# Performance work log

Hardware: AMD Instinct MI355X
Metric: run time of the kernel (lower is better)

Reference implementation:

```python
import jax, jax.numpy as jnp
import numpy as np

N_HEADS = 8
MAX_PARTS = 8
TOKENS_PER_PART = 64
NUM_BLOCKS = 6
D_MODEL = 256
LN_EPS = 1e-5


def layernorm(x, w, b):
    mu = jnp.mean(x, axis=-1, keepdims=True)
    var = jnp.var(x, axis=-1, keepdims=True)
    return (x - mu) * jax.lax.rsqrt(var + LN_EPS) * w + b


def mha(q, k, v, in_w, in_b, out_w, out_b):
    # torch nn.MultiheadAttention: packed in_proj [3D, D], out_proj [D, D]
    D = q.shape[-1]
    dh = D // N_HEADS
    wq, wk, wv = in_w[:D], in_w[D:2 * D], in_w[2 * D:]
    bq, bk, bv = in_b[:D], in_b[D:2 * D], in_b[2 * D:]
    qp = q @ wq.T + bq  # [B, Sq, D]
    kp = k @ wk.T + bk
    vp = v @ wv.T + bv
    B, Sq, _ = qp.shape
    Sk = kp.shape[1]
    qh = qp.reshape(B, Sq, N_HEADS, dh).transpose(0, 2, 1, 3)
    kh = kp.reshape(B, Sk, N_HEADS, dh).transpose(0, 2, 1, 3)
    vh = vp.reshape(B, Sk, N_HEADS, dh).transpose(0, 2, 1, 3)
    scores = jnp.einsum('bhqd,bhkd->bhqk', qh, kh) / jnp.sqrt(jnp.asarray(dh, qp.dtype))
    attn = jax.nn.softmax(scores, axis=-1)
    out = jnp.einsum('bhqk,bhkd->bhqd', attn, vh)
    out = out.transpose(0, 2, 1, 3).reshape(B, Sq, D)
    return out @ out_w.T + out_b


def setup_inputs() -> dict:
    key = jax.random.key(0)
    ks = jax.random.split(key, 16)
    s = 0.02
    return {
        'feat': jax.random.normal(ks[0], (64, 49, 512), jnp.float32),
        'img_proj_w': jax.random.normal(ks[1], (256, 512), jnp.float32) * s,
        'img_proj_b': jnp.zeros((256,), jnp.float32),
        'init_part_tokens': jax.random.normal(ks[2], (512, 256), jnp.float32),
        'part_id_emb': jax.random.normal(ks[3], (8, 256), jnp.float32),
        'local_in_w': jax.random.normal(ks[4], (768, 256), jnp.float32) * s,
        'local_in_b': jnp.zeros((768,), jnp.float32),
        'local_out_w': jax.random.normal(ks[5], (256, 256), jnp.float32) * s,
        'local_out_b': jnp.zeros((256,), jnp.float32),
        'cross_in_w': jax.random.normal(ks[6], (768, 256), jnp.float32) * s,
        'cross_in_b': jnp.zeros((768,), jnp.float32),
        'cross_out_w': jax.random.normal(ks[7], (256, 256), jnp.float32) * s,
        'cross_out_b': jnp.zeros((256,), jnp.float32),
        'norm1_w': jnp.ones((6, 256), jnp.float32),
        'norm1_b': jnp.zeros((6, 256), jnp.float32),
        'norm2_w': jnp.ones((6, 256), jnp.float32),
        'norm2_b': jnp.zeros((6, 256), jnp.float32),
        'coord_w': jax.random.normal(ks[8], (3, 256), jnp.float32) * s,
        'coord_b': jnp.zeros((3,), jnp.float32),
    }


def reference(feat, img_proj_w, img_proj_b, init_part_tokens, part_id_emb,
              local_in_w, local_in_b, local_out_w, local_out_b,
              cross_in_w, cross_in_b, cross_out_w, cross_out_b,
              norm1_w, norm1_b, norm2_w, norm2_b, coord_w, coord_b):
    B = feat.shape[0]
    P, T, D = MAX_PARTS, TOKENS_PER_PART, D_MODEL
    img_tokens = feat @ img_proj_w.T + img_proj_b  # [B, 49, D]
    # broadcast part-id embedding over tokens_per_part
    pid = jnp.repeat(part_id_emb, T, axis=0)  # [P*T, D]
    st = jnp.broadcast_to(init_part_tokens + pid, (B, P * T, D))
    for i in range(NUM_BLOCKS):
        # block-diagonal local attention: fold parts into batch dim
        parts = st.reshape(B * P, T, D)
        local = mha(parts, parts, parts, local_in_w, local_in_b, local_out_w, local_out_b)
        local = local.reshape(B, P * T, D)
        st = layernorm(st + local, norm1_w[i], norm1_b[i])
        cross = mha(st, img_tokens, img_tokens, cross_in_w, cross_in_b, cross_out_w, cross_out_b)
        st = layernorm(st + cross, norm2_w[i], norm2_b[i])
    coords = st @ coord_w.T + coord_b
    return coords.reshape(B, P, T, 3)
```

## Files before the change

kernel.cpp:

```cpp
#include <hip/hip_runtime.h>
#include <hip/hip_bf16.h>


#define B_     64
#define P_     8
#define T_     64
#define S_     512
#define D_     256
#define H_     8
#define DH_    32
#define NIMG_  49
#define M_ST   32768
#define M_IMG  3136
#define OSTR   264

#define AS1 __attribute__((address_space(1)))
#define AS3 __attribute__((address_space(3)))

typedef short bf16x8 __attribute__((ext_vector_type(8)));
typedef float f32x4  __attribute__((ext_vector_type(4)));

__device__ inline uint f2b_pk(float x, float y) {
    uint bx = __float_as_uint(x), by = __float_as_uint(y);
    bx = (bx + 0x7FFFu + ((bx >> 16) & 1u)) >> 16;
    by = (by + 0x7FFFu + ((by >> 16) & 1u)) >> 16;
    return bx | (by << 16);
}
__device__ inline ushort f2b(float x) {
    uint b = __float_as_uint(x);
    return (ushort)((b + 0x7FFFu + ((b >> 16) & 1u)) >> 16);
}
__device__ inline float b2f(ushort u) {
    return __uint_as_float(((uint)u) << 16);
}

__global__ __launch_bounds__(256) void cvt_bf16x4(
    const float4* __restrict__ in, uint2* __restrict__ out, int n4)
{
    int i = blockIdx.x * 256 + threadIdx.x;
    if (i < n4) {
        float4 v = in[i];
        out[i] = make_uint2(f2b_pk(v.x, v.y), f2b_pk(v.z, v.w));
    }
}

__global__ __launch_bounds__(256) void gemm_bf16(
    const ushort* __restrict__ A,
    const ushort* __restrict__ W,
    const float*  __restrict__ bias,
    ushort*       __restrict__ C,
    int M, int N, int K)
{
    __shared__ ushort smem[128 * 128];
    ushort* Asm = smem;
    ushort* Bsm = smem + 4096;

    const int tid  = threadIdx.x;
    const int lane = tid & 63;
    const int wave = tid >> 6;
    const int wr = wave >> 1, wc = wave & 1;
    const int row0 = blockIdx.x * 128, col0 = blockIdx.y * 128;

    f32x4 acc[4][4] = {};

    const int skc = (tid & 3) * 8;
    const int sr0 = tid >> 2;
    const int fr  = lane & 15;
    const int g   = lane >> 4;

    for (int k0 = 0; k0 < K; k0 += 32) {
        #pragma unroll
        for (int i = 0; i < 2; ++i) {
            const int r = sr0 + i * 64;
            const int e = (tid + i * 256) * 8;
            int ra = row0 + r; if (ra >= M) ra = M - 1;
            __builtin_amdgcn_global_load_lds(
                (const AS1 void*)(A + (size_t)ra * K + k0 + skc),
                (AS3 void*)&Asm[e], 16, 0, 0);
            __builtin_amdgcn_global_load_lds(
                (const AS1 void*)(W + (size_t)(col0 + r) * K + k0 + skc),
                (AS3 void*)&Bsm[e], 16, 0, 0);
        }
        __syncthreads();

        bf16x8 af[4], bf[4];
        #pragma unroll
        for (int i = 0; i < 4; ++i)
            af[i] = *reinterpret_cast<const bf16x8*>(&Asm[(wr * 64 + i * 16 + fr) * 32 + g * 8]);
        #pragma unroll
        for (int j = 0; j < 4; ++j)
            bf[j] = *reinterpret_cast<const bf16x8*>(&Bsm[(wc * 64 + j * 16 + fr) * 32 + g * 8]);
        #pragma unroll
        for (int i = 0; i < 4; ++i)
            #pragma unroll
            for (int j = 0; j < 4; ++j)
                acc[i][j] = __builtin_amdgcn_mfma_f32_16x16x32_bf16(
                    af[i], bf[j], acc[i][j], 0, 0, 0);
        __syncthreads();
    }

    float bn[4];
    #pragma unroll
    for (int j = 0; j < 4; ++j) bn[j] = bias[col0 + wc * 64 + j * 16 + fr];

    #pragma unroll
    for (int i = 0; i < 4; ++i)
        #pragma unroll
        for (int j = 0; j < 4; ++j)
            #pragma unroll
            for (int r = 0; r < 4; ++r)
                smem[(wr * 64 + i * 16 + g * 4 + r) * 128 + wc * 64 + j * 16 + fr] =
                    f2b(acc[i][j][r] + bn[j]);
    __syncthreads();

    #pragma unroll
    for (int it = 0; it < 8; ++it) {
        const int elem = (it * 256 + tid) * 8;
        const int lrow = elem >> 7, lcol = elem & 127;
        const int m = row0 + lrow;
        if (m < M)
            *reinterpret_cast<uint4*>(&C[(size_t)m * N + col0 + lcol]) =
                *reinterpret_cast<const uint4*>(&smem[elem]);
    }
}

__global__ __launch_bounds__(256) void gemm_bf16_a32(
    const float*  __restrict__ A,
    const ushort* __restrict__ W,
    const float*  __restrict__ bias,
    ushort*       __restrict__ C,
    int M, int N, int K)
{
    __shared__ ushort smem[128 * 128];
    ushort* Asm = smem;
    ushort* Bsm = smem + 4096;

    const int tid  = threadIdx.x;
    const int lane = tid & 63;
    const int wave = tid >> 6;
    const int wr = wave >> 1, wc = wave & 1;
    const int row0 = blockIdx.x * 128, col0 = blockIdx.y * 128;

    f32x4 acc[4][4] = {};

    const int skc = (tid & 3) * 8;
    const int sr0 = tid >> 2;
    const int fr  = lane & 15;
    const int g   = lane >> 4;

    for (int k0 = 0; k0 < K; k0 += 32) {
        #pragma unroll
        for (int i = 0; i < 2; ++i) {
            const int r = sr0 + i * 64;
            const int e = (tid + i * 256) * 8;
            int ra = row0 + r; if (ra >= M) ra = M - 1;
            const float* ga = A + (size_t)ra * K + k0 + skc;
            float4 v0 = *reinterpret_cast<const float4*>(ga);
            float4 v1 = *reinterpret_cast<const float4*>(ga + 4);
            uint4 pk;
            pk.x = f2b_pk(v0.x, v0.y);
            pk.y = f2b_pk(v0.z, v0.w);
            pk.z = f2b_pk(v1.x, v1.y);
            pk.w = f2b_pk(v1.z, v1.w);
            *reinterpret_cast<uint4*>(&Asm[e]) = pk;
            __builtin_amdgcn_global_load_lds(
                (const AS1 void*)(W + (size_t)(col0 + r) * K + k0 + skc),
                (AS3 void*)&Bsm[e], 16, 0, 0);
        }
        __syncthreads();

        bf16x8 af[4], bf[4];
        #pragma unroll
        for (int i = 0; i < 4; ++i)
            af[i] = *reinterpret_cast<const bf16x8*>(&Asm[(wr * 64 + i * 16 + fr) * 32 + g * 8]);
        #pragma unroll
        for (int j = 0; j < 4; ++j)
            bf[j] = *reinterpret_cast<const bf16x8*>(&Bsm[(wc * 64 + j * 16 + fr) * 32 + g * 8]);
        #pragma unroll
        for (int i = 0; i < 4; ++i)
            #pragma unroll
            for (int j = 0; j < 4; ++j)
                acc[i][j] = __builtin_amdgcn_mfma_f32_16x16x32_bf16(
                    af[i], bf[j], acc[i][j], 0, 0, 0);
        __syncthreads();
    }

    float bn[4];
    #pragma unroll
    for (int j = 0; j < 4; ++j) bn[j] = bias[col0 + wc * 64 + j * 16 + fr];

    #pragma unroll
    for (int i = 0; i < 4; ++i)
        #pragma unroll
        for (int j = 0; j < 4; ++j)
            #pragma unroll
            for (int r = 0; r < 4; ++r)
                smem[(wr * 64 + i * 16 + g * 4 + r) * 128 + wc * 64 + j * 16 + fr] =
                    f2b(acc[i][j][r] + bn[j]);
    __syncthreads();

    #pragma unroll
    for (int it = 0; it < 8; ++it) {
        const int elem = (it * 256 + tid) * 8;
        const int lrow = elem >> 7, lcol = elem & 127;
        const int m = row0 + lrow;
        if (m < M)
            *reinterpret_cast<uint4*>(&C[(size_t)m * N + col0 + lcol]) =
                *reinterpret_cast<const uint4*>(&smem[elem]);
    }
}

__global__ __launch_bounds__(512, 4) void gemm_bf16_big(
    const ushort* __restrict__ A,
    const ushort* __restrict__ W,
    const float*  __restrict__ bias,
    ushort*       __restrict__ C,
    int N, int K)
{
    __shared__ ushort smem[16384];
    ushort* Asm = smem;
    ushort* Bsm = smem + 8192;

    const int tid  = threadIdx.x;
    const int lane = tid & 63;
    const int wave = tid >> 6;
    const int wr = wave >> 1, wc = wave & 1;
    const int row0 = blockIdx.x * 256, col0 = blockIdx.y * 128;

    f32x4 acc[4][4] = {};
    const int skc = (tid & 3) * 8;
    const int sr0 = tid >> 2;
    const int fr  = lane & 15;
    const int g   = lane >> 4;

    for (int k0 = 0; k0 < K; k0 += 32) {
        #pragma unroll
        for (int i = 0; i < 2; ++i) {
            const int r = sr0 + i * 128;
            __builtin_amdgcn_global_load_lds(
                (const AS1 void*)(A + (size_t)(row0 + r) * K + k0 + skc),
                (AS3 void*)&Asm[(tid + i * 512) * 8], 16, 0, 0);
        }
        __builtin_amdgcn_global_load_lds(
            (const AS1 void*)(W + (size_t)(col0 + sr0) * K + k0 + skc),
            (AS3 void*)&Bsm[tid * 8], 16, 0, 0);
        __syncthreads();

        bf16x8 af[4], bf[4];
        #pragma unroll
        for (int i = 0; i < 4; ++i)
            af[i] = *reinterpret_cast<const bf16x8*>(&Asm[(wr * 64 + i * 16 + fr) * 32 + g * 8]);
        #pragma unroll
        for (int j = 0; j < 4; ++j)
            bf[j] = *reinterpret_cast<const bf16x8*>(&Bsm[(wc * 64 + j * 16 + fr) * 32 + g * 8]);
        #pragma unroll
        for (int i = 0; i < 4; ++i)
            #pragma unroll
            for (int j = 0; j < 4; ++j)
                acc[i][j] = __builtin_amdgcn_mfma_f32_16x16x32_bf16(
                    af[i], bf[j], acc[i][j], 0, 0, 0);
        __syncthreads();
    }

    float bn[4];
    #pragma unroll
    for (int j = 0; j < 4; ++j) bn[j] = bias[col0 + wc * 64 + j * 16 + fr];

    #pragma unroll
    for (int h2 = 0; h2 < 2; ++h2) {
        if ((wr >> 1) == h2) {
            const int lwr = wr & 1;
            #pragma unroll
            for (int i = 0; i < 4; ++i)
                #pragma unroll
                for (int j = 0; j < 4; ++j)
                    #pragma unroll
                    for (int r = 0; r < 4; ++r)
                        smem[(lwr * 64 + i * 16 + g * 4 + r) * 128 + wc * 64 + j * 16 + fr] =
                            f2b(acc[i][j][r] + bn[j]);
        }
        __syncthreads();
        #pragma unroll
        for (int it = 0; it < 4; ++it) {
            const int elem = (it * 512 + tid) * 8;
            const int lrow = elem >> 7, lcol = elem & 127;
            *reinterpret_cast<uint4*>(
                &C[(size_t)(row0 + h2 * 128 + lrow) * N + col0 + lcol]) =
                *reinterpret_cast<const uint4*>(&smem[elem]);
        }
        __syncthreads();
    }
}

template<int CROSS>
__global__ __launch_bounds__(256) void attn_oln(
    const ushort* __restrict__ qsrc,
    const ushort* __restrict__ ksrc,
    const ushort* __restrict__ vsrc,
    const ushort* __restrict__ W,
    const float*  __restrict__ bias,
    ushort*       __restrict__ stb,
    const float*  __restrict__ lnw,
    const float*  __restrict__ lnb)
{
    constexpr int QSTR = CROSS ? 256 : 768;
    constexpr int KSTR = CROSS ? 512 : 768;

    const int bid = blockIdx.x;
    int qrow0, krow0;
    if (CROSS) { qrow0 = (bid >> 3) * 512 + (bid & 7) * 64; krow0 = (bid >> 3) * 49; }
    else       { qrow0 = bid * 64; krow0 = bid * 64; }

    __shared__ ushort P_lds[4][64][72];
    __shared__ ushort Vt_lds[4][32][72];
    __shared__ float  redS[64][4];
    __shared__ float  redS2[64][4];
    ushort* Os = &P_lds[0][0][0];

    const int tid = threadIdx.x;
    const int w = tid >> 6, l = tid & 63;
    const int fr = l & 15, g = l >> 4;
    ushort (*P)[72]  = P_lds[w];
    ushort (*Vt)[72] = Vt_lds[w];

    f32x4 o2[2][4][2] = {};

    #pragma unroll
    for (int hh = 0; hh < 2; ++hh) {
        const int h = w + hh * 4;
        const int hoff = h * 32;

        bf16x8 kf[4], qf[4];
        #pragma unroll
        for (int i = 0; i < 4; ++i) {
            int t = 16 * i + fr;
            if (CROSS && t > 48) t = 48;
            kf[i] = *reinterpret_cast<const bf16x8*>(
                ksrc + (size_t)(krow0 + t) * KSTR + hoff + g * 8);
        }
        #pragma unroll
        for (int j = 0; j < 4; ++j)
            qf[j] = *reinterpret_cast<const bf16x8*>(
                qsrc + (size_t)(qrow0 + 16 * j + fr) * QSTR + hoff + g * 8);

        #pragma unroll
        for (int t2 = 0; t2 < 2; ++t2) {
            const int task = t2 * 64 + l;
            const int rp = task >> 2, cg = task & 3;
            int r0 = 2 * rp, r1 = r0 + 1;
            if (CROSS) { if (r0 > 48) r0 = 48; if (r1 > 48) r1 = 48; }
            const uint4 a = *reinterpret_cast<const uint4*>(
                vsrc + (size_t)(krow0 + r0) * KSTR + hoff + cg * 8);
            const uint4 b = *reinterpret_cast<const uint4*>(
                vsrc + (size_t)(krow0 + r1) * KSTR + hoff + cg * 8);
            const uint ac[4] = {a.x, a.y, a.z, a.w};
            const uint bc[4] = {b.x, b.y, b.z, b.w};
            #pragma unroll
            for (int k = 0; k < 4; ++k) {
                uint lo = (ac[k] & 0xFFFFu) | (bc[k] << 16);
                uint hi = (ac[k] >> 16)     | (bc[k] & 0xFFFF0000u);
                *reinterpret_cast<uint*>(&Vt[cg * 8 + 2 * k][2 * rp])     = lo;
                *reinterpret_cast<uint*>(&Vt[cg * 8 + 2 * k + 1][2 * rp]) = hi;
            }
        }

        f32x4 st_[4][4];
        #pragma unroll
        for (int i = 0; i < 4; ++i)
            #pragma unroll
            for (int j = 0; j < 4; ++j) {
                f32x4 z = {};
                st_[i][j] = __builtin_amdgcn_mfma_f32_16x16x32_bf16(
                    kf[i], qf[j], z, 0, 0, 0);
                st_[i][j] *= 0.17677669529663689f;
            }
        if (CROSS) {
            #pragma unroll
            for (int j = 0; j < 4; ++j)
                #pragma unroll
                for (int r = 0; r < 4; ++r)
                    if (r > 0 || g > 0) st_[3][j][r] = -1e30f;
        }

        #pragma unroll
        for (int j = 0; j < 4; ++j) {
            float mx = -1e30f;
            #pragma unroll
            for (int i = 0; i < 4; ++i)
                #pragma unroll
                for (int r = 0; r < 4; ++r) mx = fmaxf(mx, st_[i][j][r]);
            mx = fmaxf(mx, __shfl_xor(mx, 16));
            mx = fmaxf(mx, __shfl_xor(mx, 32));
            float sm = 0.f;
            #pragma unroll
            for (int i = 0; i < 4; ++i)
                #pragma unroll
                for (int r = 0; r < 4; ++r) {
                    float p = __expf(st_[i][j][r] - mx);
                    st_[i][j][r] = p;
                    sm += p;
                }
            sm += __shfl_xor(sm, 16);
            sm += __shfl_xor(sm, 32);
            const float inv = 1.f / sm;
            const int q = 16 * j + fr;
            #pragma unroll
            for (int i = 0; i < 4; ++i) {
                uint lo = f2b_pk(st_[i][j][0] * inv, st_[i][j][1] * inv);
                uint hi = f2b_pk(st_[i][j][2] * inv, st_[i][j][3] * inv);
                *reinterpret_cast<uint2*>(&P[q][16 * i + 4 * g]) = make_uint2(lo, hi);
            }
        }

        __syncthreads();

        #pragma unroll
        for (int s = 0; s < 2; ++s) {
            bf16x8 pa[4], vb[2];
            #pragma unroll
            for (int i = 0; i < 4; ++i)
                pa[i] = *reinterpret_cast<const bf16x8*>(&P[16 * i + fr][32 * s + 8 * g]);
            #pragma unroll
            for (int j2 = 0; j2 < 2; ++j2)
                vb[j2] = *reinterpret_cast<const bf16x8*>(&Vt[16 * j2 + fr][32 * s + 8 * g]);
            #pragma unroll
            for (int i = 0; i < 4; ++i)
                #pragma unroll
                for (int j2 = 0; j2 < 2; ++j2)
                    o2[hh][i][j2] = __builtin_amdgcn_mfma_f32_16x16x32_bf16(
                        pa[i], vb[j2], o2[hh][i][j2], 0, 0, 0);
        }
    }

    __syncthreads();

    #pragma unroll
    for (int hh = 0; hh < 2; ++hh)
        #pragma unroll
        for (int i = 0; i < 4; ++i)
            #pragma unroll
            for (int j2 = 0; j2 < 2; ++j2)
                #pragma unroll
                for (int r = 0; r < 4; ++r)
                    Os[(16 * i + 4 * g + r) * OSTR + hh * 128 + w * 32 + 16 * j2 + fr] =
                        f2b(o2[hh][i][j2][r]);
    __syncthreads();

    f32x4 acc[4][4] = {};
    #pragma unroll
    for (int k0i = 0; k0i < 8; ++k0i) {
        const int k0 = k0i * 32;
        bf16x8 af[4], bf[4];
        #pragma unroll
        for (int j = 0; j < 4; ++j)
            bf[j] = *reinterpret_cast<const bf16x8*>(
                W + (size_t)(w * 64 + j * 16 + fr) * 256 + k0 + g * 8);
        #pragma unroll
        for (int i = 0; i < 4; ++i)
            af[i] = *reinterpret_cast<const bf16x8*>(&Os[(i * 16 + fr) * OSTR + k0 + g * 8]);
        #pragma unroll
        for (int i = 0; i < 4; ++i)
            #pragma unroll
            for (int j = 0; j < 4; ++j)
                acc[i][j] = __builtin_amdgcn_mfma_f32_16x16x32_bf16(
                    af[i], bf[j], acc[i][j], 0, 0, 0);
    }

    int   col[4]; float bv[4], wv[4], lb[4];
    #pragma unroll
    for (int j = 0; j < 4; ++j) {
        col[j] = w * 64 + j * 16 + fr;
        bv[j]  = bias[col[j]];
        wv[j]  = lnw[col[j]];
        lb[j]  = lnb[col[j]];
    }

    const int row0 = qrow0;

    #pragma unroll
    for (int i = 0; i < 4; ++i)
        #pragma unroll
        for (int r = 0; r < 4; ++r) {
            const int rl = i * 16 + g * 4 + r;
            const size_t rb = (size_t)(row0 + rl) * 256;
            float s = 0.f, s2 = 0.f;
            #pragma unroll
            for (int j = 0; j < 4; ++j) {
                float x = acc[i][j][r] + bv[j] + b2f(stb[rb + col[j]]);
                acc[i][j][r] = x;
                s += x; s2 += x * x;
            }
            #pragma unroll
            for (int o = 1; o < 16; o <<= 1) {
                s  += __shfl_xor(s, o);
                s2 += __shfl_xor(s2, o);
            }
            if (fr == 0) { redS[rl][w] = s; redS2[rl][w] = s2; }
        }
    __syncthreads();

    #pragma unroll
    for (int i = 0; i < 4; ++i)
        #pragma unroll
        for (int r = 0; r < 4; ++r) {
            const int rl = i * 16 + g * 4 + r;
            const float ts  = redS[rl][0] + redS[rl][1] + redS[rl][2] + redS[rl][3];
            const float ts2 = redS2[rl][0] + redS2[rl][1] + redS2[rl][2] + redS2[rl][3];
            const float mean = ts * (1.f / 256.f);
            const float var  = ts2 * (1.f / 256.f) - mean * mean;
            const float rs   = rsqrtf(var + 1e-5f);
            #pragma unroll
            for (int j = 0; j < 4; ++j) {
                const float y = (acc[i][j][r] - mean) * rs * wv[j] + lb[j];
                Os[rl * OSTR + col[j]] = f2b(y);
            }
        }
    __syncthreads();

    #pragma unroll
    for (int it = 0; it < 8; ++it) {
        const int e = it * 256 + tid;
        const int lrow = e >> 5, lcol = (e & 31) * 8;
        *reinterpret_cast<uint4*>(&stb[(size_t)(row0 + lrow) * 256 + lcol]) =
            *reinterpret_cast<const uint4*>(&Os[lrow * OSTR + lcol]);
    }
}

__global__ __launch_bounds__(256) void init_st(
    ushort* __restrict__ stb,
    const float* __restrict__ init_tokens, const float* __restrict__ pid_emb)
{
    int i = blockIdx.x * 256 + threadIdx.x;
    int c = i & 63;
    int s = (i >> 6) & 511;
    int p = s >> 6;
    float4 v = *reinterpret_cast<const float4*>(&init_tokens[s * 256 + c * 4]);
    float4 e = *reinterpret_cast<const float4*>(&pid_emb[p * 256 + c * 4]);
    v.x += e.x; v.y += e.y; v.z += e.z; v.w += e.w;
    *reinterpret_cast<uint2*>(&stb[(size_t)i * 4]) =
        make_uint2(f2b_pk(v.x, v.y), f2b_pk(v.z, v.w));
}

__global__ __launch_bounds__(256) void coord_head(
    const ushort* __restrict__ stb, const float* __restrict__ w,
    const float* __restrict__ b, float* __restrict__ out)
{
    const int row = blockIdx.x * 8 + (threadIdx.x >> 5);
    const int l   = threadIdx.x & 31;
    const ushort* x = stb + (size_t)row * 256 + l * 8;
    uint4 xv = *reinterpret_cast<const uint4*>(x);
    float xf[8];
    const uint xc[4] = {xv.x, xv.y, xv.z, xv.w};
    #pragma unroll
    for (int k = 0; k < 4; ++k) {
        xf[2*k]   = __uint_as_float(xc[k] << 16);
        xf[2*k+1] = __uint_as_float(xc[k] & 0xFFFF0000u);
    }
    float acc[3];
    #pragma unroll
    for (int n = 0; n < 3; ++n) {
        const float* wn = w + n * 256 + l * 8;
        float4 w0 = *reinterpret_cast<const float4*>(wn);
        float4 w1 = *reinterpret_cast<const float4*>(wn + 4);
        acc[n] = xf[0]*w0.x + xf[1]*w0.y + xf[2]*w0.z + xf[3]*w0.w
               + xf[4]*w1.x + xf[5]*w1.y + xf[6]*w1.z + xf[7]*w1.w;
    }
    #pragma unroll
    for (int o = 16; o; o >>= 1)
        #pragma unroll
        for (int n = 0; n < 3; ++n) acc[n] += __shfl_xor(acc[n], o);
    if (l == 0) {
        #pragma unroll
        for (int n = 0; n < 3; ++n) out[(size_t)row * 3 + n] = acc[n] + b[n];
    }
}

extern "C" void kernel_launch(void* const* d_in, const int* in_sizes, int n_in,
                              void* d_out, int out_size, void* d_ws, size_t ws_size,
                              hipStream_t stream)
{
    const float* feat             = (const float*)d_in[0];
    const float* img_proj_w      = (const float*)d_in[1];
    const float* img_proj_b      = (const float*)d_in[2];
    const float* init_part_tokens = (const float*)d_in[3];
    const float* part_id_emb     = (const float*)d_in[4];
    const float* local_in_w      = (const float*)d_in[5];
    const float* local_in_b      = (const float*)d_in[6];
    const float* local_out_w     = (const float*)d_in[7];
    const float* local_out_b     = (const float*)d_in[8];
    const float* cross_in_w      = (const float*)d_in[9];
    const float* cross_in_b      = (const float*)d_in[10];
    const float* cross_out_w     = (const float*)d_in[11];
    const float* cross_out_b     = (const float*)d_in[12];
    const float* norm1_w         = (const float*)d_in[13];
    const float* norm1_b         = (const float*)d_in[14];
    const float* norm2_w         = (const float*)d_in[15];
    const float* norm2_b         = (const float*)d_in[16];
    const float* coord_w         = (const float*)d_in[17];
    const float* coord_b         = (const float*)d_in[18];
    float* out = (float*)d_out;

    ushort* stb  = (ushort*)d_ws;
    ushort* big  = stb  + (size_t)M_ST * D_;
    ushort* kv   = big  + (size_t)M_ST * 3 * D_;
    ushort* img  = kv   + (size_t)M_IMG * 512;
    ushort* lw_in  = img   + (size_t)M_IMG * D_;
    ushort* lw_out = lw_in  + 768 * 256;
    ushort* cw_in  = lw_out + 256 * 256;
    ushort* cw_out = cw_in  + 768 * 256;
    ushort* iw     = cw_out + 256 * 256;

    cvt_bf16x4<<<768*256/4/256, 256, 0, stream>>>((const float4*)local_in_w,  (uint2*)lw_in,  768*256/4);
    cvt_bf16x4<<<256*256/4/256, 256, 0, stream>>>((const float4*)local_out_w, (uint2*)lw_out, 256*256/4);
    cvt_bf16x4<<<768*256/4/256, 256, 0, stream>>>((const float4*)cross_in_w,  (uint2*)cw_in,  768*256/4);
    cvt_bf16x4<<<256*256/4/256, 256, 0, stream>>>((const float4*)cross_out_w, (uint2*)cw_out, 256*256/4);
    cvt_bf16x4<<<256*512/4/256, 256, 0, stream>>>((const float4*)img_proj_w,  (uint2*)iw,     256*512/4);

    gemm_bf16_a32<<<dim3((M_IMG+127)/128, 2), 256, 0, stream>>>(
        feat, iw, img_proj_b, img, M_IMG, 256, 512);
    gemm_bf16<<<dim3((M_IMG+127)/128, 4), 256, 0, stream>>>(
        img, cw_in + 256*256, cross_in_b + 256, kv, M_IMG, 512, 256);
    init_st<<<M_ST * D_ / 4 / 256, 256, 0, stream>>>(stb, init_part_tokens, part_id_emb);

    for (int i = 0; i < 6; ++i) {
        gemm_bf16_big<<<dim3(M_ST/256, 6), 512, 0, stream>>>(stb, lw_in, local_in_b, big, 768, 256);
        attn_oln<0><<<512, 256, 0, stream>>>(big, big + 256, big + 512,
                                             lw_out, local_out_b, stb,
                                             norm1_w + i*256, norm1_b + i*256);
        gemm_bf16_big<<<dim3(M_ST/256, 2), 512, 0, stream>>>(stb, cw_in, cross_in_b, big, 256, 256);
        attn_oln<1><<<512, 256, 0, stream>>>(big, kv, kv + 256,
                                             cw_out, cross_out_b, stb,
                                             norm2_w + i*256, norm2_b + i*256);
    }

    coord_head<<<M_ST / 8, 256, 0, stream>>>(stb, coord_w, coord_b, out);
}
```

Measured before the change: 665.0 us.

## Fuse cross-attention Q projection into the attention kernel

```diff
diff --git a/kernel.cpp b/kernel.cpp
--- a/kernel.cpp
+++ b/kernel.cpp
@@ -297,6 +297,8 @@
     const ushort* __restrict__ qsrc,
     const ushort* __restrict__ ksrc,
     const ushort* __restrict__ vsrc,
+    const ushort* __restrict__ qw,
+    const float*  __restrict__ qb,
     const ushort* __restrict__ W,
     const float*  __restrict__ bias,
     ushort*       __restrict__ stb,
@@ -323,6 +325,56 @@
     ushort (*P)[72]  = P_lds[w];
     ushort (*Vt)[72] = Vt_lds[w];
 
+    bf16x8 qfA[2][4];
+    if constexpr (CROSS) {
+        f32x4 aq[4][4] = {};
+        #pragma unroll
+        for (int k0i = 0; k0i < 8; ++k0i) {
+            const int k0 = k0i * 32;
+            bf16x8 af[4], bf[4];
+            #pragma unroll
+            for (int i = 0; i < 4; ++i)
+                af[i] = *reinterpret_cast<const bf16x8*>(
+                    qsrc + (size_t)(qrow0 + i * 16 + fr) * 256 + k0 + g * 8);
+            #pragma unroll
+            for (int j = 0; j < 4; ++j)
+                bf[j] = *reinterpret_cast<const bf16x8*>(
+                    qw + (size_t)(w * 64 + j * 16 + fr) * 256 + k0 + g * 8);
+            #pragma unroll
+            for (int i = 0; i < 4; ++i)
+                #pragma unroll
+                for (int j = 0; j < 4; ++j)
+                    aq[i][j] = __builtin_amdgcn_mfma_f32_16x16x32_bf16(
+                        af[i], bf[j], aq[i][j], 0, 0, 0);
+        }
+        float bqv[4];
+        #pragma unroll
+        for (int j = 0; j < 4; ++j) bqv[j] = qb[w * 64 + j * 16 + fr];
+        #pragma unroll
+        for (int i = 0; i < 4; ++i)
+            #pragma unroll
+            for (int j = 0; j < 4; ++j)
+                #pragma unroll
+                for (int r = 0; r < 4; ++r)
+                    Os[(i * 16 + g * 4 + r) * OSTR + w * 64 + j * 16 + fr] =
+                        f2b(aq[i][j][r] + bqv[j]);
+        __syncthreads();
+        #pragma unroll
+        for (int hh = 0; hh < 2; ++hh)
+            #pragma unroll
+            for (int j = 0; j < 4; ++j)
+                qfA[hh][j] = *reinterpret_cast<const bf16x8*>(
+                    &Os[(16 * j + fr) * OSTR + (w + hh * 4) * 32 + g * 8]);
+        __syncthreads();
+    } else {
+        #pragma unroll
+        for (int hh = 0; hh < 2; ++hh)
+            #pragma unroll
+            for (int j = 0; j < 4; ++j)
+                qfA[hh][j] = *reinterpret_cast<const bf16x8*>(
+                    qsrc + (size_t)(qrow0 + 16 * j + fr) * QSTR + (w + hh * 4) * 32 + g * 8);
+    }
+
     f32x4 o2[2][4][2] = {};
 
     #pragma unroll
@@ -330,7 +382,7 @@
         const int h = w + hh * 4;
         const int hoff = h * 32;
 
-        bf16x8 kf[4], qf[4];
+        bf16x8 kf[4];
         #pragma unroll
         for (int i = 0; i < 4; ++i) {
             int t = 16 * i + fr;
@@ -338,10 +390,6 @@
             kf[i] = *reinterpret_cast<const bf16x8*>(
                 ksrc + (size_t)(krow0 + t) * KSTR + hoff + g * 8);
         }
-        #pragma unroll
-        for (int j = 0; j < 4; ++j)
-            qf[j] = *reinterpret_cast<const bf16x8*>(
-                qsrc + (size_t)(qrow0 + 16 * j + fr) * QSTR + hoff + g * 8);
 
         #pragma unroll
         for (int t2 = 0; t2 < 2; ++t2) {
@@ -371,7 +419,7 @@
             for (int j = 0; j < 4; ++j) {
                 f32x4 z = {};
                 st_[i][j] = __builtin_amdgcn_mfma_f32_16x16x32_bf16(
-                    kf[i], qf[j], z, 0, 0, 0);
+                    kf[i], qfA[hh][j], z, 0, 0, 0);
                 st_[i][j] *= 0.17677669529663689f;
             }
         if (CROSS) {
@@ -625,10 +673,11 @@
     for (int i = 0; i < 6; ++i) {
         gemm_bf16_big<<<dim3(M_ST/256, 6), 512, 0, stream>>>(stb, lw_in, local_in_b, big, 768, 256);
         attn_oln<0><<<512, 256, 0, stream>>>(big, big + 256, big + 512,
+                                             nullptr, nullptr,
                                              lw_out, local_out_b, stb,
                                              norm1_w + i*256, norm1_b + i*256);
-        gemm_bf16_big<<<dim3(M_ST/256, 2), 512, 0, stream>>>(stb, cw_in, cross_in_b, big, 256, 256);
-        attn_oln<1><<<512, 256, 0, stream>>>(big, kv, kv + 256,
+        attn_oln<1><<<512, 256, 0, stream>>>(stb, kv, kv + 256,
+                                             cw_in, cross_in_b,
                                              cw_out, cross_out_b, stb,
                                              norm2_w + i*256, norm2_b + i*256);
     }
```

Result: no change. 672.4 us (+1.1%).
